# Optimization experiments

Measured on AMD Instinct MI355X. Metric: run time of the kernel, lower is better.

## Reference

```python
import jax, jax.numpy as jnp
import numpy as np

# HiLo config: dim=384, num_heads=12, alpha=0.5, window_size=2, qkv_bias=False
DIM = 384
N_HEADS = 12
HEAD_DIM = DIM // N_HEADS            # 32
L_HEADS = int(N_HEADS * 0.5)         # 6
H_HEADS = N_HEADS - L_HEADS          # 6
L_DIM = L_HEADS * HEAD_DIM           # 192
H_DIM = H_HEADS * HEAD_DIM           # 192
WS = 2
SCALE = HEAD_DIM ** -0.5
B, H, W = 2, 96, 96


def setup_inputs() -> dict:
    key = jax.random.key(0)
    ks = jax.random.split(key, 8)
    s = 0.02
    return {
        "x": jax.random.normal(ks[0], (B, DIM, H, W), jnp.float32),
        # weights stored [in, out]; linears have no bias except the two proj layers
        "Wh_qkv": jax.random.normal(ks[1], (DIM, H_DIM * 3), jnp.float32) * s,
        "Wh_proj": jax.random.normal(ks[2], (H_DIM, H_DIM), jnp.float32) * s,
        "bh_proj": jnp.zeros((H_DIM,), jnp.float32),
        "Wl_q": jax.random.normal(ks[3], (DIM, L_DIM), jnp.float32) * s,
        "Wl_kv": jax.random.normal(ks[4], (DIM, L_DIM * 2), jnp.float32) * s,
        "Wl_proj": jax.random.normal(ks[5], (L_DIM, L_DIM), jnp.float32) * s,
        "bl_proj": jnp.zeros((L_DIM,), jnp.float32),
    }


def _hifi(x, Wh_qkv, Wh_proj, bh_proj):
    # x: [B, H, W, C] -> windowed local attention over WS x WS windows
    Bx, Hx, Wx, C = x.shape
    hg, wg = Hx // WS, Wx // WS
    G, n = hg * wg, WS * WS
    xw = x.reshape(Bx, hg, WS, wg, WS, C).transpose(0, 1, 3, 2, 4, 5).reshape(Bx, G, n, C)
    qkv = (xw @ Wh_qkv).reshape(Bx, G, n, 3, H_HEADS, HEAD_DIM)
    qkv = qkv.transpose(3, 0, 1, 4, 2, 5)          # [3, B, G, h, n, d]
    q, k, v = qkv[0], qkv[1], qkv[2]
    attn = jnp.einsum('bghnd,bghmd->bghnm', q, k) * SCALE
    attn = jax.nn.softmax(attn, axis=-1)
    out = jnp.einsum('bghnm,bghmd->bghnd', attn, v)  # [B, G, h, n, d]
    out = out.transpose(0, 1, 3, 2, 4).reshape(Bx, hg, wg, WS, WS, H_DIM)
    out = out.transpose(0, 1, 3, 2, 4, 5).reshape(Bx, Hx, Wx, H_DIM)
    return out @ Wh_proj + bh_proj


def _lofi(x, Wl_q, Wl_kv, Wl_proj, bl_proj):
    # x: [B, H, W, C] -> queries from all tokens, K/V from avg-pooled tokens
    Bx, Hx, Wx, C = x.shape
    N = Hx * Wx
    q = (x.reshape(Bx, N, C) @ Wl_q).reshape(Bx, N, L_HEADS, HEAD_DIM).transpose(0, 2, 1, 3)
    # AvgPool2d(WS, WS) on channels-last layout
    xp = x.reshape(Bx, Hx // WS, WS, Wx // WS, WS, C).mean(axis=(2, 4))  # [B, hg, wg, C]
    M = (Hx // WS) * (Wx // WS)
    kv = (xp.reshape(Bx, M, C) @ Wl_kv).reshape(Bx, M, 2, L_HEADS, HEAD_DIM)
    kv = kv.transpose(2, 0, 3, 1, 4)               # [2, B, h, M, d]
    k, v = kv[0], kv[1]
    attn = jnp.einsum('bhnd,bhmd->bhnm', q, k) * SCALE
    attn = jax.nn.softmax(attn, axis=-1)
    out = jnp.einsum('bhnm,bhmd->bhnd', attn, v)   # [B, h, N, d]
    out = out.transpose(0, 2, 1, 3).reshape(Bx, Hx, Wx, L_DIM)
    return out @ Wl_proj + bl_proj


def reference(x, Wh_qkv, Wh_proj, bh_proj, Wl_q, Wl_kv, Wl_proj, bl_proj):
    Bx, C, Hx, Wx = x.shape
    xc = x.transpose(0, 2, 3, 1)                   # [B, H, W, C]
    hi = _hifi(xc, Wh_qkv, Wh_proj, bh_proj)       # [B, H, W, H_DIM]
    lo = _lofi(xc, Wl_q, Wl_kv, Wl_proj, bl_proj)  # [B, H, W, L_DIM]
    out = jnp.concatenate((hi, lo), axis=-1).reshape(Bx, Hx * Wx, C)
    return out.transpose(0, 2, 1).reshape(Bx, C, Hx, Wx)
```

## Files before the change

kernel.cpp:

```cpp
#include <hip/hip_runtime.h>

typedef unsigned short u16;

#define DEV static __device__ __forceinline__

DEV float bf2f(u16 v) { unsigned x = ((unsigned)v) << 16; return __uint_as_float(x); }
DEV u16 f2bf(float f) {
    unsigned x = __float_as_uint(f);
    unsigned r = (x + 0x7fffu + ((x >> 16) & 1u)) >> 16;
    return (u16)r;
}

constexpr int BATCH = 2;
constexpr int CH    = 384;
constexpr int HH    = 96;
constexpr int WW    = 96;
constexpr int NTOK  = HH * WW;
constexpr int GW    = 48;
constexpr int G     = GW * GW;
constexpr int HEADS = 6;
constexpr int NT    = G / 64;
constexpr float SCALE = 0.17677669529663687f;
constexpr float QKSCALE = 0.25503497438034225f;

typedef __attribute__((ext_vector_type(8)))  short short8v;
typedef __attribute__((ext_vector_type(4)))  float f32x4;
typedef __attribute__((ext_vector_type(16))) float f32x16;

DEV f32x4 mfma16(short8v a, short8v b, f32x4 c) {
    return __builtin_amdgcn_mfma_f32_16x16x32_bf16(a, b, c, 0, 0, 0);
}
DEV f32x16 mfma32(short8v a, short8v b, f32x16 c) {
    return __builtin_amdgcn_mfma_f32_32x32x16_bf16(a, b, c, 0, 0, 0);
}

DEV unsigned cvtpk_bf16(float a, float b) {
    unsigned r;
    asm("v_cvt_pk_bf16_f32 %0, %1, %2" : "=v"(r) : "v"(a), "v"(b));
    return r;
}

DEV float exp2fast(float x) {
    float r;
    asm("v_exp_f32 %0, %1" : "=v"(r) : "v"(x));
    return r;
}

DEV void permswap(unsigned& a, unsigned& b) {
    asm("v_permlane32_swap_b32 %0, %1" : "+v"(a), "+v"(b));
}

DEV void unpack8(uint4 u, float* f) {
    unsigned a0 = u.x, a1 = u.y, a2 = u.z, a3 = u.w;
    f[0] = bf2f((u16)(a0 & 0xffffu)); f[1] = bf2f((u16)(a0 >> 16));
    f[2] = bf2f((u16)(a1 & 0xffffu)); f[3] = bf2f((u16)(a1 >> 16));
    f[4] = bf2f((u16)(a2 & 0xffffu)); f[5] = bf2f((u16)(a2 >> 16));
    f[6] = bf2f((u16)(a3 & 0xffffu)); f[7] = bf2f((u16)(a3 >> 16));
}

__global__ __launch_bounds__(256) void prep(const float* __restrict__ x,
        const float* __restrict__ W0, const float* __restrict__ W1,
        const float* __restrict__ W2, const float* __restrict__ W3,
        const float* __restrict__ W4,
        u16* __restrict__ xT, u16* __restrict__ xpool,
        u16* __restrict__ D0, u16* __restrict__ D1, u16* __restrict__ D2,
        u16* __restrict__ D3, u16* __restrict__ D4) {
    __shared__ float ts[32][33];
    int tid = threadIdx.x;
    int id = blockIdx.x;
    if (id < 6912) {
        int cx = id % 288, cy = (id / 288) % 12, b = id / 3456;
        int c0 = cx * 32, r0 = cy * 32;
        int row = tid >> 3, cg = tid & 7;
        float4 v = *(const float4*)&x[(size_t)b * CH * NTOK + (size_t)(r0 + row) * NTOK + c0 + cg * 4];
        ts[row][cg * 4 + 0] = v.x; ts[row][cg * 4 + 1] = v.y;
        ts[row][cg * 4 + 2] = v.z; ts[row][cg * 4 + 3] = v.w;
        __syncthreads();
        int cc = tid >> 3, rg = tid & 7;
        uint2 u;
        u.x = (unsigned)f2bf(ts[rg * 4 + 0][cc]) | ((unsigned)f2bf(ts[rg * 4 + 1][cc]) << 16);
        u.y = (unsigned)f2bf(ts[rg * 4 + 2][cc]) | ((unsigned)f2bf(ts[rg * 4 + 3][cc]) << 16);
        *(uint2*)&xT[(size_t)b * NTOK * CH + (size_t)(c0 + cc) * CH + r0 + rg * 4] = u;
    } else if (id < 8640) {
        int t = id - 6912;
        int mx = t % 72, cy = (t / 72) % 12, b = t / 864;
        int m0 = mx * 32, c0 = cy * 32;
        int cc = tid >> 3, mg = tid & 7;
        const float* xb = x + ((size_t)b * CH + c0 + cc) * NTOK;
        #pragma unroll
        for (int i = 0; i < 4; i++) {
            int m = m0 + mg * 4 + i;
            int gy = m / GW, gx = m - gy * GW;
            const float* p = xb + gy * 2 * WW + gx * 2;
            ts[cc][mg * 4 + i] = 0.25f * (p[0] + p[1] + p[WW] + p[WW + 1]);
        }
        __syncthreads();
        int mm = tid >> 3, cg = tid & 7;
        uint2 u;
        u.x = (unsigned)f2bf(ts[cg * 4 + 0][mm]) | ((unsigned)f2bf(ts[cg * 4 + 1][mm]) << 16);
        u.y = (unsigned)f2bf(ts[cg * 4 + 2][mm]) | ((unsigned)f2bf(ts[cg * 4 + 3][mm]) << 16);
        *(uint2*)&xpool[((size_t)b * G + m0 + mm) * CH + c0 + cg * 4] = u;
    } else {
        int wid = id - 8640;
        const float* src; u16* dst; int R, C; float scale; int cx, cy;
        if (wid < 216)      { src = W0; dst = D0; R = 384; C = 576; scale = 1.f;     cx = wid % 18; cy = wid / 18; }
        else if (wid < 288) { src = W1; dst = D1; R = 384; C = 192; scale = QKSCALE; int t = wid - 216; cx = t % 6;  cy = t / 6; }
        else if (wid < 432) { src = W2; dst = D2; R = 384; C = 384; scale = 1.f;     int t = wid - 288; cx = t % 12; cy = t / 12; }
        else if (wid < 468) { src = W3; dst = D3; R = 192; C = 192; scale = 1.f;     int t = wid - 432; cx = t % 6;  cy = t / 6; }
        else                { src = W4; dst = D4; R = 192; C = 192; scale = 1.f;     int t = wid - 468; cx = t % 6;  cy = t / 6; }
        int c0 = cx * 32, r0 = cy * 32;
        int row = tid >> 3, cg = tid & 7;
        float4 v = *(const float4*)&src[(size_t)(r0 + row) * C + c0 + cg * 4];
        ts[row][cg * 4 + 0] = v.x; ts[row][cg * 4 + 1] = v.y;
        ts[row][cg * 4 + 2] = v.z; ts[row][cg * 4 + 3] = v.w;
        __syncthreads();
        int cc = tid >> 3, rg = tid & 7;
        uint2 u;
        u.x = (unsigned)f2bf(scale * ts[rg * 4 + 0][cc]) | ((unsigned)f2bf(scale * ts[rg * 4 + 1][cc]) << 16);
        u.y = (unsigned)f2bf(scale * ts[rg * 4 + 2][cc]) | ((unsigned)f2bf(scale * ts[rg * 4 + 3][cc]) << 16);
        *(uint2*)&dst[(size_t)(c0 + cc) * R + r0 + rg * 4] = u;
    }
}

template<int K>
DEV void gemm64_body(const u16* __restrict__ Pr, const u16* __restrict__ Qr,
                     u16* pt, u16* qt, int tid, f32x4 acc[4]) {
    int w = tid >> 6, lane = tid & 63;
    int l15 = lane & 15, q4 = lane >> 4;
    int lr = tid >> 2, lc = tid & 3;
    const f32x4 zero4 = {0.f, 0.f, 0.f, 0.f};
    acc[0] = zero4; acc[1] = zero4; acc[2] = zero4; acc[3] = zero4;
    uint4 pv = *(const uint4*)&Pr[(size_t)lr * K + lc * 8];
    uint4 qv = *(const uint4*)&Qr[(size_t)lr * K + lc * 8];
    for (int k0 = 0; k0 < K; k0 += 32) {
        __syncthreads();
        *(uint4*)&pt[lr * 40 + lc * 8] = pv;
        *(uint4*)&qt[lr * 40 + lc * 8] = qv;
        if (k0 + 32 < K) {
            pv = *(const uint4*)&Pr[(size_t)lr * K + k0 + 32 + lc * 8];
            qv = *(const uint4*)&Qr[(size_t)lr * K + k0 + 32 + lc * 8];
        }
        __syncthreads();
        short8v pa = *(const short8v*)&pt[(w * 16 + l15) * 40 + q4 * 8];
        #pragma unroll
        for (int qg = 0; qg < 4; qg++) {
            short8v qb = *(const short8v*)&qt[(qg * 16 + l15) * 40 + q4 * 8];
            acc[qg] = mfma16(pa, qb, acc[qg]);
        }
    }
}

__global__ __launch_bounds__(256) void gemm_all(const u16* __restrict__ WT768,
        const u16* __restrict__ xT, const u16* __restrict__ WlkT,
        const u16* __restrict__ WvT, const u16* __restrict__ xpool,
        u16* __restrict__ tokf, u16* __restrict__ kF, u16* __restrict__ vF) {
    __shared__ u16 pt[64 * 40];
    __shared__ u16 qt[64 * 40];
    int tid = threadIdx.x, id = blockIdx.x;
    int w = tid >> 6, lane = tid & 63, l15 = lane & 15, q4 = lane >> 4;
    f32x4 acc[4];
    if (id < 3456) {
        int px = id % 12, qy = (id / 12) % 144, b = id / 1728;
        gemm64_body<CH>(WT768 + (size_t)px * 64 * CH,
                        xT + ((size_t)b * NTOK + qy * 64) * CH, pt, qt, tid, acc);
        #pragma unroll
        for (int qg = 0; qg < 4; qg++) {
            int q = qy * 64 + qg * 16 + l15;
            int p = px * 64 + w * 16 + q4 * 4;
            uint2 pk;
            pk.x = (unsigned)f2bf(acc[qg][0]) | ((unsigned)f2bf(acc[qg][1]) << 16);
            pk.y = (unsigned)f2bf(acc[qg][2]) | ((unsigned)f2bf(acc[qg][3]) << 16);
            *(uint2*)&tokf[((size_t)b * NTOK + q) * 768 + p] = pk;
        }
    } else if (id < 3672) {
        int u = id - 3456;
        int px = u % 3, qy = (u / 3) % 36, b = u / 108;
        gemm64_body<CH>(WlkT + (size_t)px * 64 * CH,
                        xpool + ((size_t)b * G + qy * 64) * CH, pt, qt, tid, acc);
        #pragma unroll
        for (int qg = 0; qg < 4; qg++) {
            int m = qy * 64 + qg * 16 + l15;
            int d = px * 64 + w * 16 + q4 * 4;
            int h = d >> 5, dh = (d >> 4) & 1, hi2 = (d >> 3) & 1;
            int kh = (m >> 5) & 1, tile = m >> 6, slot = kh * 2 + dh;
            int lane2 = (m & 31) + 32 * hi2;
            size_t addr = ((((size_t)(b * HEADS + h) * NT + tile) * 4 + slot) * 64 + lane2) * 8 + (d & 7);
            uint2 pk;
            pk.x = (unsigned)f2bf(acc[qg][0]) | ((unsigned)f2bf(acc[qg][1]) << 16);
            pk.y = (unsigned)f2bf(acc[qg][2]) | ((unsigned)f2bf(acc[qg][3]) << 16);
            *(uint2*)&kF[addr] = pk;
        }
    } else {
        int u = id - 3672;
        int px = u % 36, qy = (u / 36) % 3, b = u / 108;
        gemm64_body<CH>(xpool + ((size_t)b * G + px * 64) * CH,
                        WvT + (size_t)qy * 64 * CH, pt, qt, tid, acc);
        #pragma unroll
        for (int qg = 0; qg < 4; qg++) {
            int jj = qy * 64 + qg * 16 + l15;
            int m = px * 64 + w * 16 + q4 * 4;
            int h = jj >> 5, d31 = jj & 31;
            int tile = m >> 6, slot = (m >> 4) & 3, hi2 = (m >> 3) & 1;
            int lane2 = d31 + 32 * hi2;
            size_t addr = ((((size_t)(b * HEADS + h) * NT + tile) * 4 + slot) * 64 + lane2) * 8 + (m & 7);
            uint2 pk;
            pk.x = (unsigned)f2bf(acc[qg][0]) | ((unsigned)f2bf(acc[qg][1]) << 16);
            pk.y = (unsigned)f2bf(acc[qg][2]) | ((unsigned)f2bf(acc[qg][3]) << 16);
            *(uint2*)&vF[addr] = pk;
        }
    }
}

__global__ __launch_bounds__(128) void mega_attn(const u16* __restrict__ tokf,
        const u16* __restrict__ kF, const u16* __restrict__ vF,
        u16* __restrict__ hi_ao, u16* __restrict__ lo_ao) {
    __shared__ float smem[2560];
    int tid = threadIdx.x;
    int id = blockIdx.x;
    const f32x16 zero16 = {0.f,0.f,0.f,0.f,0.f,0.f,0.f,0.f,0.f,0.f,0.f,0.f,0.f,0.f,0.f,0.f};

    if (id < 3456) {
        int lane = tid & 63, khalf = tid >> 6;
        int l31 = lane & 31, hi = lane >> 5;
        int qt = id % 288, h = (id / 288) % HEADS, b = id / 1728;

        short8v qb0, qb1;
        {
            int nq = qt * 32 + l31;
            const u16* qrow = &tokf[((size_t)b * NTOK + nq) * 768 + 576 + h * 32];
            qb0 = *(const short8v*)&qrow[hi * 8];
            qb1 = *(const short8v*)&qrow[16 + hi * 8];
        }
        f32x16 accO = zero16;
        float lrow = 0.f;

        const u16* kbh = kF + ((size_t)(b * HEADS + h) * NT + khalf * 18) * 2048 + lane * 8;
        const u16* vbh = vF + ((size_t)(b * HEADS + h) * NT + khalf * 18) * 2048 + lane * 8;

        short8v kb[4], vb[4];
        #pragma unroll
        for (int sl = 0; sl < 4; sl++) {
            kb[sl] = *(const short8v*)&kbh[sl * 512];
            vb[sl] = *(const short8v*)&vbh[sl * 512];
        }

        for (int t = 0; t < 18; t++) {
            int tn = (t + 1 < 18) ? t + 1 : t;
            short8v nk[4], nv[4];
            {
                const u16* kn = kbh + (size_t)tn * 2048;
                const u16* vn = vbh + (size_t)tn * 2048;
                #pragma unroll
                for (int sl = 0; sl < 4; sl++) {
                    nk[sl] = *(const short8v*)&kn[sl * 512];
                    nv[sl] = *(const short8v*)&vn[sl * 512];
                }
            }
            f32x16 s0 = mfma32(kb[0], qb0, zero16);
            s0 = mfma32(kb[1], qb1, s0);
            f32x16 s1 = mfma32(kb[2], qb0, zero16);
            s1 = mfma32(kb[3], qb1, s1);

            unsigned pk[2][8];
            float ls = 0.f;
            #pragma unroll
            for (int kh = 0; kh < 2; kh++) {
                const f32x16& sv = kh ? s1 : s0;
                #pragma unroll
                for (int i = 0; i < 8; i++) {
                    float e0 = exp2fast(sv[2 * i]);
                    float e1 = exp2fast(sv[2 * i + 1]);
                    ls += e0 + e1;
                    pk[kh][i] = cvtpk_bf16(e0, e1);
                }
                permswap(pk[kh][0], pk[kh][2]);
                permswap(pk[kh][1], pk[kh][3]);
                permswap(pk[kh][4], pk[kh][6]);
                permswap(pk[kh][5], pk[kh][7]);
            }
            lrow += ls;
            #pragma unroll
            for (int kt = 0; kt < 4; kt++) {
                union { unsigned u[4]; short8v v; } pa;
                pa.u[0] = pk[kt >> 1][(kt & 1) * 4 + 0];
                pa.u[1] = pk[kt >> 1][(kt & 1) * 4 + 1];
                pa.u[2] = pk[kt >> 1][(kt & 1) * 4 + 2];
                pa.u[3] = pk[kt >> 1][(kt & 1) * 4 + 3];
                accO = mfma32(pa.v, vb[kt], accO);
            }
            #pragma unroll
            for (int sl = 0; sl < 4; sl++) { kb[sl] = nk[sl]; vb[sl] = nv[sl]; }
        }

        float* mAcc = smem;
        float* mL = smem + 1024;
        if (khalf == 1) {
            #pragma unroll
            for (int r = 0; r < 16; r++) mAcc[lane * 16 + r] = accO[r];
            mL[lane] = lrow;
        }
        __syncthreads();
        if (khalf == 0) {
            #pragma unroll
            for (int r = 0; r < 16; r++) accO[r] += mAcc[lane * 16 + r];
            lrow += mL[lane];
            float l = lrow + __shfl_xor(lrow, 32);
            float inv = 1.0f / l;
            #pragma unroll
            for (int r = 0; r < 16; r++) {
                int qr = (r & 3) + 8 * (r >> 2) + 4 * hi;
                float ir = __shfl(inv, qr);
                int n = qt * 32 + qr;
                lo_ao[((size_t)b * NTOK + n) * 192 + h * 32 + l31] = f2bf(accO[r] * ir);
            }
        }
    } else {
        int bg = id - 3456;
        int b = bg / G, g = bg % G;
        int gy = g / GW, gx = g % GW;
        float (*sq)[576] = (float(*)[576])smem;
        float* satt = smem + 2304;
        float* sp   = smem + 2400;

        for (int c = tid; c < 288; c += 128) {
            int t = c / 72, j8 = c - t * 72;
            int n = (gy * 2 + (t >> 1)) * WW + gx * 2 + (t & 1);
            uint4 u = *(const uint4*)&tokf[((size_t)b * NTOK + n) * 768 + j8 * 8];
            unpack8(u, &sq[t][j8 * 8]);
        }
        __syncthreads();

        if (tid < 96) {
            int h = tid >> 4, tq = (tid >> 2) & 3, tm = tid & 3;
            const float* qp = &sq[tq][h * 32];
            const float* kp = &sq[tm][192 + h * 32];
            float s0 = 0, s1 = 0, s2 = 0, s3 = 0;
            #pragma unroll
            for (int d = 0; d < 32; d += 4) {
                s0 += qp[d] * kp[d];
                s1 += qp[d + 1] * kp[d + 1];
                s2 += qp[d + 2] * kp[d + 2];
                s3 += qp[d + 3] * kp[d + 3];
            }
            satt[h * 16 + tq * 4 + tm] = (s0 + s1 + s2 + s3) * SCALE;
        }
        __syncthreads();
        if (tid < 24) {
            int h = tid >> 2, t = tid & 3;
            float l0 = satt[h * 16 + t * 4 + 0], l1 = satt[h * 16 + t * 4 + 1];
            float l2 = satt[h * 16 + t * 4 + 2], l3 = satt[h * 16 + t * 4 + 3];
            float mx = fmaxf(fmaxf(l0, l1), fmaxf(l2, l3));
            float e0 = __expf(l0 - mx), e1 = __expf(l1 - mx);
            float e2 = __expf(l2 - mx), e3 = __expf(l3 - mx);
            float inv = 1.0f / (e0 + e1 + e2 + e3);
            sp[h * 16 + t * 4 + 0] = e0 * inv; sp[h * 16 + t * 4 + 1] = e1 * inv;
            sp[h * 16 + t * 4 + 2] = e2 * inv; sp[h * 16 + t * 4 + 3] = e3 * inv;
        }
        __syncthreads();
        {
            int t = tid >> 5, d = tid & 31;
            int n = (gy * 2 + (t >> 1)) * WW + gx * 2 + (t & 1);
            u16* op = &hi_ao[((size_t)b * NTOK + n) * 192];
            #pragma unroll
            for (int h = 0; h < HEADS; h++) {
                float o = sp[h * 16 + t * 4 + 0] * sq[0][384 + h * 32 + d]
                        + sp[h * 16 + t * 4 + 1] * sq[1][384 + h * 32 + d]
                        + sp[h * 16 + t * 4 + 2] * sq[2][384 + h * 32 + d]
                        + sp[h * 16 + t * 4 + 3] * sq[3][384 + h * 32 + d];
                op[h * 32 + d] = f2bf(o);
            }
        }
    }
}

__global__ __launch_bounds__(256) void proj_both(const u16* __restrict__ hi_ao,
        const u16* __restrict__ lo_ao, const u16* __restrict__ WhpT,
        const u16* __restrict__ WlpT, const float* __restrict__ bh,
        const float* __restrict__ bl, float* __restrict__ out) {
    __shared__ u16 pt[64 * 40];
    __shared__ u16 qt[64 * 40];
    int tid = threadIdx.x;
    int z = blockIdx.z, which = z >> 1, b = z & 1;
    const u16* A = which ? lo_ao : hi_ao;
    const u16* W = which ? WlpT : WhpT;
    const float* bias = which ? bl : bh;
    int p0 = blockIdx.x * 64, q0 = blockIdx.y * 64;
    f32x4 acc[4];
    gemm64_body<192>(A + ((size_t)b * NTOK + p0) * 192, W + (size_t)q0 * 192,
                     pt, qt, tid, acc);
    int w = tid >> 6, lane = tid & 63, l15 = lane & 15, q4 = lane >> 4;
    #pragma unroll
    for (int qg = 0; qg < 4; qg++) {
        int q = q0 + qg * 16 + l15;
        int p = p0 + w * 16 + q4 * 4;
        float bb = bias[q];
        float4 o = make_float4(acc[qg][0] + bb, acc[qg][1] + bb,
                               acc[qg][2] + bb, acc[qg][3] + bb);
        *(float4*)&out[((size_t)b * CH + which * 192 + q) * NTOK + p] = o;
    }
}

extern "C" void kernel_launch(void* const* d_in, const int* in_sizes, int n_in,
                              void* d_out, int out_size, void* d_ws, size_t ws_size,
                              hipStream_t stream) {
    const float* x       = (const float*)d_in[0];
    const float* Wh_qkv  = (const float*)d_in[1];
    const float* Wh_proj = (const float*)d_in[2];
    const float* bh_proj = (const float*)d_in[3];
    const float* Wl_q    = (const float*)d_in[4];
    const float* Wl_kv   = (const float*)d_in[5];
    const float* Wl_proj = (const float*)d_in[6];
    const float* bl_proj = (const float*)d_in[7];
    float* out = (float*)d_out;

    char* ws = (char*)d_ws;
    u16*   tokf  = (u16*)ws;
    char*  ws1   = ws + (size_t)28311552;
    u16*   xT    = (u16*)ws1;
    u16*   hi_ao = (u16*)ws1;
    u16*   lo_ao = (u16*)(ws1 + 7077888);
    char*  ws2   = ws1 + (size_t)14155776;
    u16*   kF    = (u16*)ws2;
    u16*   vF    = (u16*)(ws2 + 1769472);
    char*  ws3   = ws2 + (size_t)7077888;
    u16*   xpool = (u16*)ws3;
    char*  ws4   = ws3 + (size_t)3538944;
    u16*   WT768 = (u16*)ws4;
    u16*   WlkvT = WT768 + 768 * 384;
    u16*   WhpT  = WlkvT + 384 * 384;
    u16*   WlpT  = WhpT + 192 * 192;
    u16*   WlkT  = WlkvT;
    u16*   WvT   = WlkvT + 192 * 384;

    prep<<<dim3(9144), 256, 0, stream>>>(
        x, Wh_qkv, Wl_q, Wl_kv, Wh_proj, Wl_proj,
        xT, xpool, WT768, WT768 + 576 * 384, WlkvT, WhpT, WlpT);

    gemm_all<<<dim3(3888), 256, 0, stream>>>(
        WT768, xT, WlkT, WvT, xpool, tokf, kF, vF);

    mega_attn<<<dim3(8064), 128, 0, stream>>>(tokf, kF, vF, hi_ao, lo_ao);

    proj_both<<<dim3(144, 3, 4), 256, 0, stream>>>(
        hi_ao, lo_ao, WhpT, WlpT, bh_proj, bl_proj, out);
}
```

Before: 132.3 us.

## Split lofi KV loop across four waves and compute row sums via MFMA

The mega_attn block grows from 128 to 256 threads, so each lofi block splits the 36 KV tiles across four waves (9 each) instead of two. Each wave now keeps its own exp-sum through an extra MFMA against a ones vector rather than scalar adds and shuffles. The partial results are reduced through padded shared memory, and the final normalisation uses a fast reciprocal. The explicit register double-buffer prefetch is dropped, and the hifi branch redistributes its work for 256 threads. The aim is more parallelism per query tile and less VALU work, paid for with extra MFMA issues, larger LDS use and a bigger cross-wave reduction.

```diff
diff --git a/kernel.cpp b/kernel.cpp
--- a/kernel.cpp
+++ b/kernel.cpp
@@ -43,6 +43,12 @@
 DEV float exp2fast(float x) {
     float r;
     asm("v_exp_f32 %0, %1" : "=v"(r) : "v"(x));
+    return r;
+}
+
+DEV float rcpfast(float x) {
+    float r;
+    asm("v_rcp_f32 %0, %1" : "=v"(r) : "v"(x));
     return r;
 }
 
@@ -211,18 +217,21 @@
     }
 }
 
-__global__ __launch_bounds__(128) void mega_attn(const u16* __restrict__ tokf,
+__global__ __launch_bounds__(256, 4) void mega_attn(const u16* __restrict__ tokf,
         const u16* __restrict__ kF, const u16* __restrict__ vF,
         u16* __restrict__ hi_ao, u16* __restrict__ lo_ao) {
-    __shared__ float smem[2560];
+    __shared__ float smem[6528];
     int tid = threadIdx.x;
     int id = blockIdx.x;
     const f32x16 zero16 = {0.f,0.f,0.f,0.f,0.f,0.f,0.f,0.f,0.f,0.f,0.f,0.f,0.f,0.f,0.f,0.f};
 
     if (id < 3456) {
-        int lane = tid & 63, khalf = tid >> 6;
+        int lane = tid & 63, kq = tid >> 6;
         int l31 = lane & 31, hi = lane >> 5;
         int qt = id % 288, h = (id / 288) % HEADS, b = id / 1728;
+
+        const short8v ones = {(short)0x3F80, (short)0x3F80, (short)0x3F80, (short)0x3F80,
+                              (short)0x3F80, (short)0x3F80, (short)0x3F80, (short)0x3F80};
 
         short8v qb0, qb1;
         {
@@ -231,87 +240,86 @@
             qb0 = *(const short8v*)&qrow[hi * 8];
             qb1 = *(const short8v*)&qrow[16 + hi * 8];
         }
-        f32x16 accO = zero16;
-        float lrow = 0.f;
-
-        const u16* kbh = kF + ((size_t)(b * HEADS + h) * NT + khalf * 18) * 2048 + lane * 8;
-        const u16* vbh = vF + ((size_t)(b * HEADS + h) * NT + khalf * 18) * 2048 + lane * 8;
-
-        short8v kb[4], vb[4];
-        #pragma unroll
-        for (int sl = 0; sl < 4; sl++) {
-            kb[sl] = *(const short8v*)&kbh[sl * 512];
-            vb[sl] = *(const short8v*)&vbh[sl * 512];
-        }
-
-        for (int t = 0; t < 18; t++) {
-            int tn = (t + 1 < 18) ? t + 1 : t;
-            short8v nk[4], nv[4];
-            {
-                const u16* kn = kbh + (size_t)tn * 2048;
-                const u16* vn = vbh + (size_t)tn * 2048;
+        f32x16 accO = zero16, accL = zero16;
+
+        const u16* kp = kF + ((size_t)(b * HEADS + h) * NT + kq * 9) * 2048 + lane * 8;
+        const u16* vp = vF + ((size_t)(b * HEADS + h) * NT + kq * 9) * 2048 + lane * 8;
+
+        for (int t = 0; t < 9; t++) {
+            short8v kb0 = *(const short8v*)(kp);
+            short8v kb1 = *(const short8v*)(kp + 512);
+            short8v kb2 = *(const short8v*)(kp + 1024);
+            short8v kb3 = *(const short8v*)(kp + 1536);
+            short8v vb0 = *(const short8v*)(vp);
+            short8v vb1 = *(const short8v*)(vp + 512);
+            short8v vb2 = *(const short8v*)(vp + 1024);
+            short8v vb3 = *(const short8v*)(vp + 1536);
+            kp += 2048; vp += 2048;
+
+            f32x16 s0 = mfma32(kb0, qb0, zero16);
+            s0 = mfma32(kb1, qb1, s0);
+            unsigned pk0[8];
+            #pragma unroll
+            for (int i = 0; i < 8; i++)
+                pk0[i] = cvtpk_bf16(exp2fast(s0[2 * i]), exp2fast(s0[2 * i + 1]));
+            permswap(pk0[0], pk0[2]);
+            permswap(pk0[1], pk0[3]);
+            permswap(pk0[4], pk0[6]);
+            permswap(pk0[5], pk0[7]);
+
+            f32x16 s1 = mfma32(kb2, qb0, zero16);
+            s1 = mfma32(kb3, qb1, s1);
+            unsigned pk1[8];
+            #pragma unroll
+            for (int i = 0; i < 8; i++)
+                pk1[i] = cvtpk_bf16(exp2fast(s1[2 * i]), exp2fast(s1[2 * i + 1]));
+            permswap(pk1[0], pk1[2]);
+            permswap(pk1[1], pk1[3]);
+            permswap(pk1[4], pk1[6]);
+            permswap(pk1[5], pk1[7]);
+
+            union { unsigned u[4]; short8v v; } pa;
+            pa.u[0] = pk0[0]; pa.u[1] = pk0[1]; pa.u[2] = pk0[2]; pa.u[3] = pk0[3];
+            accO = mfma32(pa.v, vb0, accO);
+            accL = mfma32(pa.v, ones, accL);
+            pa.u[0] = pk0[4]; pa.u[1] = pk0[5]; pa.u[2] = pk0[6]; pa.u[3] = pk0[7];
+            accO = mfma32(pa.v, vb1, accO);
+            accL = mfma32(pa.v, ones, accL);
+            pa.u[0] = pk1[0]; pa.u[1] = pk1[1]; pa.u[2] = pk1[2]; pa.u[3] = pk1[3];
+            accO = mfma32(pa.v, vb2, accO);
+            accL = mfma32(pa.v, ones, accL);
+            pa.u[0] = pk1[4]; pa.u[1] = pk1[5]; pa.u[2] = pk1[6]; pa.u[3] = pk1[7];
+            accO = mfma32(pa.v, vb3, accO);
+            accL = mfma32(pa.v, ones, accL);
+        }
+
+        float* mO = smem;
+        float* mL = smem + 3264;
+        if (kq) {
+            int base = (kq - 1) * 1088 + lane * 17;
+            #pragma unroll
+            for (int r = 0; r < 16; r++) {
+                mO[base + r] = accO[r];
+                mL[base + r] = accL[r];
+            }
+        }
+        __syncthreads();
+        if (kq == 0) {
+            #pragma unroll
+            for (int w2 = 0; w2 < 3; w2++) {
+                int base = w2 * 1088 + lane * 17;
                 #pragma unroll
-                for (int sl = 0; sl < 4; sl++) {
-                    nk[sl] = *(const short8v*)&kn[sl * 512];
-                    nv[sl] = *(const short8v*)&vn[sl * 512];
+                for (int r = 0; r < 16; r++) {
+                    accO[r] += mO[base + r];
+                    accL[r] += mL[base + r];
                 }
             }
-            f32x16 s0 = mfma32(kb[0], qb0, zero16);
-            s0 = mfma32(kb[1], qb1, s0);
-            f32x16 s1 = mfma32(kb[2], qb0, zero16);
-            s1 = mfma32(kb[3], qb1, s1);
-
-            unsigned pk[2][8];
-            float ls = 0.f;
-            #pragma unroll
-            for (int kh = 0; kh < 2; kh++) {
-                const f32x16& sv = kh ? s1 : s0;
-                #pragma unroll
-                for (int i = 0; i < 8; i++) {
-                    float e0 = exp2fast(sv[2 * i]);
-                    float e1 = exp2fast(sv[2 * i + 1]);
-                    ls += e0 + e1;
-                    pk[kh][i] = cvtpk_bf16(e0, e1);
-                }
-                permswap(pk[kh][0], pk[kh][2]);
-                permswap(pk[kh][1], pk[kh][3]);
-                permswap(pk[kh][4], pk[kh][6]);
-                permswap(pk[kh][5], pk[kh][7]);
-            }
-            lrow += ls;
-            #pragma unroll
-            for (int kt = 0; kt < 4; kt++) {
-                union { unsigned u[4]; short8v v; } pa;
-                pa.u[0] = pk[kt >> 1][(kt & 1) * 4 + 0];
-                pa.u[1] = pk[kt >> 1][(kt & 1) * 4 + 1];
-                pa.u[2] = pk[kt >> 1][(kt & 1) * 4 + 2];
-                pa.u[3] = pk[kt >> 1][(kt & 1) * 4 + 3];
-                accO = mfma32(pa.v, vb[kt], accO);
-            }
-            #pragma unroll
-            for (int sl = 0; sl < 4; sl++) { kb[sl] = nk[sl]; vb[sl] = nv[sl]; }
-        }
-
-        float* mAcc = smem;
-        float* mL = smem + 1024;
-        if (khalf == 1) {
-            #pragma unroll
-            for (int r = 0; r < 16; r++) mAcc[lane * 16 + r] = accO[r];
-            mL[lane] = lrow;
-        }
-        __syncthreads();
-        if (khalf == 0) {
-            #pragma unroll
-            for (int r = 0; r < 16; r++) accO[r] += mAcc[lane * 16 + r];
-            lrow += mL[lane];
-            float l = lrow + __shfl_xor(lrow, 32);
-            float inv = 1.0f / l;
             #pragma unroll
             for (int r = 0; r < 16; r++) {
                 int qr = (r & 3) + 8 * (r >> 2) + 4 * hi;
-                float ir = __shfl(inv, qr);
                 int n = qt * 32 + qr;
-                lo_ao[((size_t)b * NTOK + n) * 192 + h * 32 + l31] = f2bf(accO[r] * ir);
+                lo_ao[((size_t)b * NTOK + n) * 192 + h * 32 + l31] =
+                    f2bf(accO[r] * rcpfast(accL[r]));
             }
         }
     } else {
@@ -322,7 +330,7 @@
         float* satt = smem + 2304;
         float* sp   = smem + 2400;
 
-        for (int c = tid; c < 288; c += 128) {
+        for (int c = tid; c < 288; c += 256) {
             int t = c / 72, j8 = c - t * 72;
             int n = (gy * 2 + (t >> 1)) * WW + gx * 2 + (t & 1);
             uint4 u = *(const uint4*)&tokf[((size_t)b * NTOK + n) * 768 + j8 * 8];
@@ -358,11 +366,12 @@
         }
         __syncthreads();
         {
-            int t = tid >> 5, d = tid & 31;
+            int t = tid >> 6, hp = (tid >> 5) & 1, d = tid & 31;
             int n = (gy * 2 + (t >> 1)) * WW + gx * 2 + (t & 1);
             u16* op = &hi_ao[((size_t)b * NTOK + n) * 192];
             #pragma unroll
-            for (int h = 0; h < HEADS; h++) {
+            for (int hh = 0; hh < 3; hh++) {
+                int h = hp * 3 + hh;
                 float o = sp[h * 16 + t * 4 + 0] * sq[0][384 + h * 32 + d]
                         + sp[h * 16 + t * 4 + 1] * sq[1][384 + h * 32 + d]
                         + sp[h * 16 + t * 4 + 2] * sq[2][384 + h * 32 + d]
@@ -439,7 +448,7 @@
     gemm_all<<<dim3(3888), 256, 0, stream>>>(
         WT768, xT, WlkT, WvT, xpool, tokf, kF, vF);
 
-    mega_attn<<<dim3(8064), 128, 0, stream>>>(tokf, kF, vF, hi_ao, lo_ao);
+    mega_attn<<<dim3(8064), 256, 0, stream>>>(tokf, kF, vF, hi_ao, lo_ao);
 
     proj_both<<<dim3(144, 3, 4), 256, 0, stream>>>(
         hi_ao, lo_ao, WhpT, WlpT, bh_proj, bl_proj, out);
```

Result: faster. 125.0 us (-5.5%).
